# Optimization experiments

Measured on AMD Instinct MI355X. Metric: run time of the kernel, lower is better.

## Reference

```python
import jax, jax.numpy as jnp
import numpy as np

V, D, H, L, F, S, B = 32000, 1024, 16, 4, 4096, 1024, 2
THETA = 10000.0
EPS = 1e-5


def rmsnorm(x, w):
    # faithful to source: rms = sqrt(mean(x^2)) + eps (eps OUTSIDE the sqrt)
    rms = jnp.sqrt(jnp.mean(x * x, axis=-1, keepdims=True)) + EPS
    return (x / rms) * w


def rope(x, pos):
    # x: [B, H, S, dk]; rotate interleaved even/odd pairs
    dk = x.shape[-1]
    inv_freq = 1.0 / (THETA ** (jnp.arange(0, dk, 2, dtype=jnp.float32) / dk))
    ang = pos[:, None].astype(jnp.float32) * inv_freq[None, :]  # [S, dk/2]
    cos, sin = jnp.cos(ang), jnp.sin(ang)
    x1, x2 = x[..., ::2], x[..., 1::2]
    r1 = x1 * cos - x2 * sin
    r2 = x1 * sin + x2 * cos
    return jnp.stack([r1, r2], axis=-1).reshape(x.shape)


def setup_inputs() -> dict:
    key = jax.random.key(0)
    ks = jax.random.split(key, 12)
    s_attn = np.sqrt(2.0 / (D + D)).astype(np.float32)
    s_ffn = np.sqrt(2.0 / (F + D)).astype(np.float32)
    s_head = np.sqrt(2.0 / (V + D)).astype(np.float32)
    return {
        "token_ids": jax.random.randint(ks[0], (B, S), 0, V),
        "tok_emb": jax.random.normal(ks[1], (V, D), jnp.float32),
        "lm_head_w": jax.random.normal(ks[2], (V, D), jnp.float32) * s_head,
        "ln_final_w": jnp.ones((D,), jnp.float32),
        "q_w": jax.random.normal(ks[3], (L, D, D), jnp.float32) * s_attn,
        "k_w": jax.random.normal(ks[4], (L, D, D), jnp.float32) * s_attn,
        "v_w": jax.random.normal(ks[5], (L, D, D), jnp.float32) * s_attn,
        "o_w": jax.random.normal(ks[6], (L, D, D), jnp.float32) * s_attn,
        "ln1_w": jnp.ones((L, D), jnp.float32),
        "ln2_w": jnp.ones((L, D), jnp.float32),
        "w1": jax.random.normal(ks[7], (L, F, D), jnp.float32) * s_ffn,
        "w2": jax.random.normal(ks[8], (L, D, F), jnp.float32) * s_ffn,
        "w3": jax.random.normal(ks[9], (L, F, D), jnp.float32) * s_ffn,
    }


def reference(token_ids, tok_emb, lm_head_w, ln_final_w, q_w, k_w, v_w, o_w,
              ln1_w, ln2_w, w1, w2, w3):
    b, s = token_ids.shape
    dk = D // H
    scale = 1.0 / np.sqrt(dk).astype(np.float32)
    pos = jnp.arange(s)
    causal = jnp.tril(jnp.ones((s, s), dtype=bool))  # mask[i,j] = i >= j
    x = tok_emb[token_ids]  # [B, S, D]

    for l in range(L):
        # attention block with RoPE
        h = rmsnorm(x, ln1_w[l])
        q = (h @ q_w[l].T).reshape(b, s, H, dk).transpose(0, 2, 1, 3)
        k = (h @ k_w[l].T).reshape(b, s, H, dk).transpose(0, 2, 1, 3)
        v = (h @ v_w[l].T).reshape(b, s, H, dk).transpose(0, 2, 1, 3)
        q = rope(q, pos)
        k = rope(k, pos)
        scores = jnp.einsum('bhqd,bhkd->bhqk', q, k) * scale
        scores = jnp.where(causal, scores, -jnp.inf)
        attn = jax.nn.softmax(scores, axis=-1)
        o = jnp.einsum('bhqk,bhkd->bhqd', attn, v)
        o = o.transpose(0, 2, 1, 3).reshape(b, s, D)
        x = x + o @ o_w[l].T

        # SwiGLU FFN block
        h2 = rmsnorm(x, ln2_w[l])
        xw = h2 @ w1[l].T                       # [B, S, F]
        swish = xw * jax.nn.sigmoid(xw)
        x = x + (swish * (h2 @ w3[l].T)) @ w2[l].T

    x = rmsnorm(x, ln_final_w)
    return x @ lm_head_w.T  # logits [B, S, V]
```

## Files before the change

### kernel.cpp

```cpp
#include <hip/hip_runtime.h>
#include <math.h>

#define V_SZ 32000
#define D_SZ 1024
#define H_SZ 16
#define L_SZ 4
#define F_SZ 4096
#define S_SZ 1024
#define B_SZ 2
#define DK 64
#define NTOK (B_SZ * S_SZ)
#define NEG_INF -3.0e38f

typedef _Float16 half8 __attribute__((ext_vector_type(8)));
typedef _Float16 half4 __attribute__((ext_vector_type(4)));
typedef float floatx4 __attribute__((ext_vector_type(4)));

__device__ __forceinline__ void gload16(const void* g, void* l) {
    __builtin_amdgcn_global_load_lds(
        (const __attribute__((address_space(1))) unsigned int*)g,
        (__attribute__((address_space(3))) unsigned int*)l, 16, 0, 0);
}

__global__ __launch_bounds__(256) void f2h4(const float* __restrict__ s0,
                                            const float* __restrict__ s1,
                                            const float* __restrict__ s2,
                                            const float* __restrict__ s3,
                                            _Float16* __restrict__ d, int n8each) {
    const int i = blockIdx.x * 256 + threadIdx.x;
    const int sel = i / n8each;
    const int off = i - sel * n8each;
    const float* s = sel == 0 ? s0 : (sel == 1 ? s1 : (sel == 2 ? s2 : s3));
    const float4 a = ((const float4*)s)[2 * off];
    const float4 b = ((const float4*)s)[2 * off + 1];
    half8 h = {(_Float16)a.x, (_Float16)a.y, (_Float16)a.z, (_Float16)a.w,
               (_Float16)b.x, (_Float16)b.y, (_Float16)b.z, (_Float16)b.w};
    ((half8*)d)[i] = h;
}

__global__ __launch_bounds__(256) void f2h3(const float* __restrict__ s0,
                                            const float* __restrict__ s1,
                                            const float* __restrict__ s2,
                                            _Float16* __restrict__ d, int n8each) {
    const int i = blockIdx.x * 256 + threadIdx.x;
    const int sel = i / n8each;
    const int off = i - sel * n8each;
    const float* s = sel == 0 ? s0 : (sel == 1 ? s1 : s2);
    const float4 a = ((const float4*)s)[2 * off];
    const float4 b = ((const float4*)s)[2 * off + 1];
    half8 h = {(_Float16)a.x, (_Float16)a.y, (_Float16)a.z, (_Float16)a.w,
               (_Float16)b.x, (_Float16)b.y, (_Float16)b.z, (_Float16)b.w};
    ((half8*)d)[i] = h;
}

__global__ __launch_bounds__(256) void f2h(const float* __restrict__ in,
                                           _Float16* __restrict__ out, int n8) {
    const int i = blockIdx.x * 256 + threadIdx.x;
    if (i >= n8) return;
    const float4 a = ((const float4*)in)[2 * i];
    const float4 b = ((const float4*)in)[2 * i + 1];
    half8 h = {(_Float16)a.x, (_Float16)a.y, (_Float16)a.z, (_Float16)a.w,
               (_Float16)b.x, (_Float16)b.y, (_Float16)b.z, (_Float16)b.w};
    ((half8*)out)[i] = h;
}

__global__ __launch_bounds__(256) void embed_kernel(const int* __restrict__ ids,
                                                    const float* __restrict__ emb,
                                                    float* __restrict__ x) {
    const int row = blockIdx.x;
    const int id = ids[row];
    const float4* src = (const float4*)(emb + (size_t)id * D_SZ);
    float4* dst = (float4*)(x + (size_t)row * D_SZ);
    dst[threadIdx.x] = src[threadIdx.x];
}

__global__ __launch_bounds__(256) void rmsnorm_kernel(const float* __restrict__ x,
                                                      const float* __restrict__ w,
                                                      _Float16* __restrict__ out) {
    const int row = blockIdx.x;
    const int tid = threadIdx.x;
    const float4 v = ((const float4*)(x + (size_t)row * D_SZ))[tid];
    float ss = v.x * v.x + v.y * v.y + v.z * v.z + v.w * v.w;
#pragma unroll
    for (int off = 32; off > 0; off >>= 1) ss += __shfl_down(ss, off, 64);
    __shared__ float red[4];
    if ((tid & 63) == 0) red[tid >> 6] = ss;
    __syncthreads();
    const float tot = red[0] + red[1] + red[2] + red[3];
    const float inv = 1.0f / (sqrtf(tot * (1.0f / (float)D_SZ)) + 1e-5f);
    const float4 wv = ((const float4*)w)[tid];
    half4 o = {(_Float16)(v.x * inv * wv.x), (_Float16)(v.y * inv * wv.y),
               (_Float16)(v.z * inv * wv.z), (_Float16)(v.w * inv * wv.w)};
    ((half4*)(out + (size_t)row * D_SZ))[tid] = o;
}

template <int EPI, bool MFAST, int TM>
__global__ __launch_bounds__(256) void hgemm(const _Float16* __restrict__ A,
                                             const _Float16* __restrict__ B,
                                             float* __restrict__ Cf,
                                             _Float16* Ch,
                                             const _Float16* AUXh,
                                             _Float16* Cq,
                                             _Float16* Ck,
                                             _Float16* Cv,
                                             int M, int N, int K) {
    constexpr int WN = (TM == 128) ? 2 : 4;
    constexpr int CW = 128 / WN;
    constexpr int FN = CW / 16;
    __shared__ __align__(16) _Float16 As[2][TM * 32];
    __shared__ __align__(16) _Float16 Bs[2][128 * 32];
    const int tid = threadIdx.x;
    const int lane = tid & 63;
    const int wave = tid >> 6;
    const int wr = (TM == 128) ? (wave >> 1) : 0;
    const int wc = (TM == 128) ? (wave & 1) : wave;
    const int l15 = lane & 15, g = lane >> 4;

    const int gm = M / TM, gn = N >> 7, nwg = gm * gn;
    const int orig = blockIdx.x;
    const int q8 = nwg >> 3, r8 = nwg & 7, xcd = orig & 7, j8 = orig >> 3;
    const int wgid = (xcd < r8 ? xcd * (q8 + 1) : r8 * (q8 + 1) + (xcd - r8) * q8) + j8;
    const int bm = MFAST ? (wgid % gm) : (wgid / gn);
    const int bn = MFAST ? (wgid / gm) : (wgid % gn);
    const int m0 = bm * TM, n0 = bn * 128;

    const int offA0 = wave * (TM * 16) + lane * 16;
    const int offA1 = offA0 + 1024;
    const int rA0 = offA0 >> 6, kA0 = offA0 & 63;
    const int rA1 = offA1 >> 6, kA1 = offA1 & 63;
    const int offB0 = wave * 2048 + lane * 16;
    const int offB1 = offB0 + 1024;
    const int rB0 = offB0 >> 6, kB0 = offB0 & 63;
    const int rB1 = offB1 >> 6, kB1 = offB1 & 63;
    const char* gA0 = (const char*)(A + (size_t)(m0 + rA0) * K) + kA0;
    const char* gA1 = (const char*)(A + (size_t)(m0 + rA1) * K) + kA1;
    const char* gB0 = (const char*)(B + (size_t)(n0 + rB0) * K) + kB0;
    const char* gB1 = (const char*)(B + (size_t)(n0 + rB1) * K) + kB1;

#define STAGE(buf)                                                     \
    do {                                                               \
        gload16(gA0, (char*)As[buf] + offA0);                          \
        if constexpr (TM == 128) gload16(gA1, (char*)As[buf] + offA1); \
        gload16(gB0, (char*)Bs[buf] + offB0);                          \
        gload16(gB1, (char*)Bs[buf] + offB1);                          \
        gA0 += 64; gA1 += 64; gB0 += 64; gB1 += 64;                    \
    } while (0)

    floatx4 acc[4][FN];
#pragma unroll
    for (int i = 0; i < 4; i++)
#pragma unroll
        for (int j = 0; j < FN; j++) acc[i][j] = 0;

    STAGE(0);
    __syncthreads();
    int cur = 0;
    for (int kk = 0; kk < K; kk += 32) {
        if (kk + 32 < K) STAGE(cur ^ 1);
        half8 aF[4], bF[FN];
#pragma unroll
        for (int i = 0; i < 4; i++)
            aF[i] = *(const half8*)&As[cur][(wr * 64 + i * 16 + l15) * 32 + g * 8];
#pragma unroll
        for (int j = 0; j < FN; j++)
            bF[j] = *(const half8*)&Bs[cur][(wc * CW + j * 16 + l15) * 32 + g * 8];
#pragma unroll
        for (int i = 0; i < 4; i++)
#pragma unroll
            for (int j = 0; j < FN; j++)
                acc[i][j] = __builtin_amdgcn_mfma_f32_16x16x32_f16(aF[i], bF[j], acc[i][j], 0, 0, 0);
        __syncthreads();
        cur ^= 1;
    }
#undef STAGE

    const int rb = m0 + wr * 64 + g * 4;
    const int cb = n0 + wc * CW + l15;
    if (EPI == 4) {
        const int sel = n0 >> 10;
        _Float16* Cx = sel == 0 ? Cq : (sel == 1 ? Ck : Cv);
        const int cb0 = cb - sel * 1024;
#pragma unroll
        for (int i = 0; i < 4; i++) {
#pragma unroll
            for (int e = 0; e < 4; e++) {
                const int row = rb + i * 16 + e;
                const int pos = row & (S_SZ - 1);
#pragma unroll
                for (int j = 0; j < FN; j++) {
                    float v = acc[i][j][e];
                    const int col = cb0 + j * 16;
                    if (sel < 2) {
                        const float p = __shfl_xor(v, 1, 64);
                        const int pi = (col & 63) >> 1;
                        const float invf = exp2f((float)pi * -0.41524101186f);
                        float sn, cs;
                        sincosf((float)pos * invf, &sn, &cs);
                        v = (col & 1) ? (p * sn + v * cs) : (v * cs - p * sn);
                    }
                    Cx[(size_t)row * 1024 + col] = (_Float16)v;
                }
            }
        }
        return;
    }
#pragma unroll
    for (int i = 0; i < 4; i++) {
#pragma unroll
        for (int e = 0; e < 4; e++) {
            const int row = rb + i * 16 + e;
#pragma unroll
            for (int j = 0; j < FN; j++) {
                const float v = acc[i][j][e];
                if (EPI == 0) {
                    Cf[(size_t)row * N + cb + j * 16] = v;
                } else if (EPI == 1) {
                    Cf[(size_t)row * N + cb + j * 16] += v;
                } else if (EPI == 2) {
                    Ch[(size_t)row * N + cb + j * 16] =
                        (_Float16)(v / (1.0f + __expf(-v)));
                } else if (EPI == 3) {
                    const size_t idx = (size_t)row * N + cb + j * 16;
                    Ch[idx] = (_Float16)((float)AUXh[idx] * v);
                }
            }
        }
    }
}

__global__ __launch_bounds__(256) void vtrans(const _Float16* __restrict__ vh,
                                              _Float16* __restrict__ vt) {
    __shared__ __align__(16) _Float16 Ls[64][80];
    const int t = threadIdx.x;
    const int s0 = blockIdx.x * 64;
    const int bh = blockIdx.y;
    const int b = bh >> 4, h = bh & 15;
#pragma unroll
    for (int p = 0; p < 2; ++p) {
        const int sl = p * 32 + (t >> 3);
        const int d = (t & 7) * 8;
        *(half8*)&Ls[sl][d] =
            *(const half8*)&vh[((size_t)b * S_SZ + s0 + sl) * D_SZ + h * 64 + d];
    }
    __syncthreads();
#pragma unroll
    for (int p = 0; p < 2; ++p) {
        const int d = p * 32 + (t >> 3);
        const int sc = (t & 7) * 8;
        half8 v;
#pragma unroll
        for (int j = 0; j < 8; ++j) v[j] = Ls[sc + j][d];
        *(half8*)&vt[((size_t)bh * 64 + d) * S_SZ + s0 + sc] = v;
    }
}

__global__ __launch_bounds__(256) void attn_mfma(const _Float16* __restrict__ qh,
                                                 const _Float16* __restrict__ kh,
                                                 const _Float16* __restrict__ vt,
                                                 _Float16* __restrict__ o) {
    __shared__ __align__(16) _Float16 Ks[2][64 * 64];
    __shared__ __align__(16) _Float16 Vs[2][64 * 64];
    __shared__ __align__(16) _Float16 Ps[4][16][88];
    const int tid = threadIdx.x;
    const int lane = tid & 63, wave = tid >> 6;
    const int l15 = lane & 15, g = lane >> 4;
    const int bx = blockIdx.x;
    const int bh = blockIdx.y;
    const int h = bh & 15;
    const size_t tokb = (size_t)(bh >> 4) * S_SZ;

    const int qt0 = bx, qt1 = 15 - bx;
    const int qb0 = qt0 * 64, qb1 = qt1 * 64;
    const int ktmax = qt1;

    const int qrow = l15 * 4 + wave;
    half8 qA0[2], qA1[2];
#pragma unroll
    for (int kk = 0; kk < 2; ++kk) {
        qA0[kk] = *(const half8*)&qh[(tokb + qb0 + qrow) * D_SZ + h * 64 + kk * 32 + g * 8];
        qA1[kk] = *(const half8*)&qh[(tokb + qb1 + qrow) * D_SZ + h * 64 + kk * 32 + g * 8];
    }

    floatx4 accO0[4], accO1[4];
#pragma unroll
    for (int s = 0; s < 4; s++) { accO0[s] = 0; accO1[s] = 0; }
    float m0_[4] = {NEG_INF, NEG_INF, NEG_INF, NEG_INF};
    float l0_[4] = {0.0f, 0.0f, 0.0f, 0.0f};
    float m1_[4] = {NEG_INF, NEG_INF, NEG_INF, NEG_INF};
    float l1_[4] = {0.0f, 0.0f, 0.0f, 0.0f};

    const char* KbB = (const char*)(kh + tokb * D_SZ + h * 64);
    const char* VbB = (const char*)(vt + (size_t)bh * 64 * S_SZ);
    const int so0 = wave * 2048 + lane * 16;
    const int so1 = so0 + 1024;
    const int r0 = so0 >> 7, c0 = (so0 >> 4) & 7;
    const int r1 = so1 >> 7, c1 = (so1 >> 4) & 7;
    const int gc0 = ((c0 ^ (r0 & 7)) << 4);
    const int gc1 = ((c1 ^ (r1 & 7)) << 4);

#define STAGEKV(buf, kt)                                                   \
    do {                                                                   \
        const size_t kvr = (size_t)(kt) * 64;                              \
        gload16(KbB + (kvr + r0) * 2048 + gc0, (char*)Ks[buf] + so0);      \
        gload16(KbB + (kvr + r1) * 2048 + gc1, (char*)Ks[buf] + so1);      \
        gload16(VbB + r0 * 2048 + kvr * 2 + gc0, (char*)Vs[buf] + so0);    \
        gload16(VbB + r1 * 2048 + kvr * 2 + gc1, (char*)Vs[buf] + so1);    \
    } while (0)

#define LDSW(arr, rr, cc) \
    (*(const half8*)&(arr)[(rr) * 64 + ((((cc) ^ ((rr) & 7))) << 3)])

    auto computeTile = [&](const half8* qA, floatx4* accO, float* m_, float* l_,
                           int qbase, int kt, bool diag, int buf) {
        const int kv0 = kt * 64;
        floatx4 accS[4];
#pragma unroll
        for (int sub = 0; sub < 4; ++sub) {
            accS[sub] = 0;
#pragma unroll
            for (int kk = 0; kk < 2; ++kk) {
                half8 kB = LDSW(Ks[buf], sub * 16 + l15, kk * 4 + g);
                accS[sub] = __builtin_amdgcn_mfma_f32_16x16x32_f16(qA[kk], kB, accS[sub], 0, 0, 0);
            }
        }
        float sv[4][4];
        float mx[4] = {NEG_INF, NEG_INF, NEG_INF, NEG_INF};
#pragma unroll
        for (int sub = 0; sub < 4; ++sub)
#pragma unroll
            for (int e = 0; e < 4; ++e) {
                float s = accS[sub][e] * 0.125f;
                if (diag && (kv0 + sub * 16 + l15 > qbase + (g * 4 + e) * 4 + wave))
                    s = NEG_INF;
                sv[sub][e] = s;
                mx[e] = fmaxf(mx[e], s);
            }
#pragma unroll
        for (int msk = 1; msk <= 8; msk <<= 1)
#pragma unroll
            for (int e = 0; e < 4; ++e)
                mx[e] = fmaxf(mx[e], __shfl_xor(mx[e], msk, 64));
        float sf[4];
#pragma unroll
        for (int e = 0; e < 4; ++e) {
            const float mn = fmaxf(m_[e], mx[e]);
            sf[e] = __expf(m_[e] - mn);
            m_[e] = mn;
        }
        float rs[4] = {0.0f, 0.0f, 0.0f, 0.0f};
#pragma unroll
        for (int sub = 0; sub < 4; ++sub)
#pragma unroll
            for (int e = 0; e < 4; ++e) {
                const float p = __expf(sv[sub][e] - m_[e]);
                sv[sub][e] = p;
                rs[e] += p;
            }
#pragma unroll
        for (int msk = 1; msk <= 8; msk <<= 1)
#pragma unroll
            for (int e = 0; e < 4; ++e)
                rs[e] += __shfl_xor(rs[e], msk, 64);
#pragma unroll
        for (int e = 0; e < 4; ++e) l_[e] = l_[e] * sf[e] + rs[e];
#pragma unroll
        for (int sub = 0; sub < 4; ++sub)
#pragma unroll
            for (int e = 0; e < 4; ++e) accO[sub][e] *= sf[e];
#pragma unroll
        for (int sub = 0; sub < 4; ++sub)
#pragma unroll
            for (int e = 0; e < 4; ++e)
                Ps[wave][g * 4 + e][sub * 16 + l15] = (_Float16)sv[sub][e];
        half8 aP[2];
        aP[0] = *(const half8*)&Ps[wave][l15][g * 8];
        aP[1] = *(const half8*)&Ps[wave][l15][32 + g * 8];
#pragma unroll
        for (int sub = 0; sub < 4; ++sub)
#pragma unroll
            for (int kk = 0; kk < 2; ++kk) {
                half8 vB = LDSW(Vs[buf], sub * 16 + l15, kk * 4 + g);
                accO[sub] = __builtin_amdgcn_mfma_f32_16x16x32_f16(aP[kk], vB, accO[sub], 0, 0, 0);
            }
    };

    STAGEKV(0, 0);
    __syncthreads();
    int cur = 0;
    for (int kt = 0; kt <= ktmax; ++kt) {
        if (kt < ktmax) STAGEKV(cur ^ 1, kt + 1);
        computeTile(qA1, accO1, m1_, l1_, qb1, kt, kt == qt1, cur);
        if (kt <= qt0)
            computeTile(qA0, accO0, m0_, l0_, qb0, kt, kt == qt0, cur);
        __syncthreads();
        cur ^= 1;
    }
#undef STAGEKV
#undef LDSW

#pragma unroll
    for (int sub = 0; sub < 4; ++sub)
#pragma unroll
        for (int e = 0; e < 4; ++e) {
            const int rr = (g * 4 + e) * 4 + wave;
            o[(tokb + qb1 + rr) * D_SZ + h * 64 + sub * 16 + l15] =
                (_Float16)(accO1[sub][e] / l1_[e]);
            o[(tokb + qb0 + rr) * D_SZ + h * 64 + sub * 16 + l15] =
                (_Float16)(accO0[sub][e] / l0_[e]);
        }
}

extern "C" void kernel_launch(void* const* d_in, const int* in_sizes, int n_in,
                              void* d_out, int out_size, void* d_ws, size_t ws_size,
                              hipStream_t stream) {
    const int*   token_ids  = (const int*)d_in[0];
    const float* tok_emb    = (const float*)d_in[1];
    const float* lm_head_w  = (const float*)d_in[2];
    const float* ln_final_w = (const float*)d_in[3];
    const float* q_w        = (const float*)d_in[4];
    const float* k_w        = (const float*)d_in[5];
    const float* v_w        = (const float*)d_in[6];
    const float* o_w        = (const float*)d_in[7];
    const float* ln1_w      = (const float*)d_in[8];
    const float* ln2_w      = (const float*)d_in[9];
    const float* w1         = (const float*)d_in[10];
    const float* w2         = (const float*)d_in[11];
    const float* w3         = (const float*)d_in[12];
    float* out = (float*)d_out;

    char* W = (char*)d_ws;
    const size_t MB = 1u << 20;
    float*    x    = (float*)(W + 0);
    _Float16* h    = (_Float16*)(W + 8 * MB);
    _Float16* ao   = (_Float16*)(W + 12 * MB);
    _Float16* wq   = (_Float16*)(W + 16 * MB);
    _Float16* wo   = wq + 3 * (1u << 20);
    _Float16* ww1  = (_Float16*)(W + 24 * MB);
    _Float16* ww3  = ww1 + (F_SZ * D_SZ);
    _Float16* ww2  = ww3 + (F_SZ * D_SZ);
    _Float16* qh   = (_Float16*)(W + 48 * MB);
    _Float16* kh   = (_Float16*)(W + 52 * MB);
    _Float16* vh   = (_Float16*)(W + 56 * MB);
    _Float16* vt   = (_Float16*)(W + 60 * MB);
    _Float16* ff1h = (_Float16*)(W + 64 * MB);
    _Float16* whead = (_Float16*)(W + 24 * MB);

    embed_kernel<<<NTOK, 256, 0, stream>>>(token_ids, tok_emb, x);

    const int nDD8 = D_SZ * D_SZ / 8;
    const int nFD8 = F_SZ * D_SZ / 8;
    const dim3 gQKV(3 * D_SZ / 128 * (NTOK / 128));
    const dim3 gD64(D_SZ / 128 * (NTOK / 64));
    const dim3 gF(F_SZ / 128 * (NTOK / 128));
    const dim3 gATT(S_SZ / 128, B_SZ * H_SZ);
    const dim3 gVT(S_SZ / 64, B_SZ * H_SZ);

    for (int l = 0; l < L_SZ; l++) {
        const size_t oDD = (size_t)l * D_SZ * D_SZ;
        const size_t oFD = (size_t)l * F_SZ * D_SZ;
        rmsnorm_kernel<<<NTOK, 256, 0, stream>>>(x, ln1_w + (size_t)l * D_SZ, h);
        f2h4<<<4 * nDD8 / 256, 256, 0, stream>>>(q_w + oDD, k_w + oDD, v_w + oDD,
                                                 o_w + oDD, wq, nDD8);
        f2h3<<<3 * nFD8 / 256, 256, 0, stream>>>(w1 + oFD, w3 + oFD, w2 + oFD,
                                                 ww1, nFD8);
        hgemm<4, true, 128><<<gQKV, 256, 0, stream>>>(h, wq, nullptr, nullptr, nullptr,
                                                      qh, kh, vh, NTOK, 3 * D_SZ, D_SZ);
        vtrans<<<gVT, 256, 0, stream>>>(vh, vt);
        attn_mfma<<<gATT, 256, 0, stream>>>(qh, kh, vt, ao);
        hgemm<1, false, 64><<<gD64, 256, 0, stream>>>(ao, wo, x, nullptr, nullptr,
                                                      nullptr, nullptr, nullptr, NTOK, D_SZ, D_SZ);
        rmsnorm_kernel<<<NTOK, 256, 0, stream>>>(x, ln2_w + (size_t)l * D_SZ, h);
        hgemm<2, true, 128><<<gF, 256, 0, stream>>>(h, ww1, nullptr, ff1h, nullptr,
                                                    nullptr, nullptr, nullptr, NTOK, F_SZ, D_SZ);
        hgemm<3, true, 128><<<gF, 256, 0, stream>>>(h, ww3, nullptr, ff1h, ff1h,
                                                    nullptr, nullptr, nullptr, NTOK, F_SZ, D_SZ);
        hgemm<1, false, 64><<<gD64, 256, 0, stream>>>(ff1h, ww2, x, nullptr, nullptr,
                                                      nullptr, nullptr, nullptr, NTOK, D_SZ, F_SZ);
    }
    rmsnorm_kernel<<<NTOK, 256, 0, stream>>>(x, ln_final_w, h);
    const int nVD8 = V_SZ * D_SZ / 8;
    f2h<<<(nVD8 + 255) / 256, 256, 0, stream>>>(lm_head_w, whead, nVD8);
    const dim3 gOUT(V_SZ / 128 * (NTOK / 128));
    hgemm<0, true, 128><<<gOUT, 256, 0, stream>>>(h, whead, out, nullptr, nullptr,
                                                  nullptr, nullptr, nullptr, NTOK, V_SZ, D_SZ);
}
```

Measured before the change: 1.286 ms.

## Merge weight conversions, fuse W1/W3 GEMMs, add occupancy hint and MFMA priority

Merges the two per-layer fp32-to-fp16 weight conversion kernels into one launch. Runs the W1 and W3 projections as a single GEMM over the concatenated weights: the first half writes swish output, the second half writes a separate fp16 buffer, and a new elementwise kernel then multiplies them. It also adds a launch_bounds minimum-occupancy hint of 5 to the GEMM and raises wave priority around the MFMA loops in attention. The extra multiply pass adds a read and write of a 2048x4096 fp16 intermediate, and the occupancy hint may force register spills.

```diff
diff --git a/kernel.cpp b/kernel.cpp
--- a/kernel.cpp
+++ b/kernel.cpp
@@ -22,30 +22,28 @@
         (__attribute__((address_space(3))) unsigned int*)l, 16, 0, 0);
 }
 
-__global__ __launch_bounds__(256) void f2h4(const float* __restrict__ s0,
+__global__ __launch_bounds__(256) void f2h7(const float* __restrict__ sq,
+                                            const float* __restrict__ sk,
+                                            const float* __restrict__ sv,
+                                            const float* __restrict__ so,
                                             const float* __restrict__ s1,
+                                            const float* __restrict__ s3,
                                             const float* __restrict__ s2,
-                                            const float* __restrict__ s3,
-                                            _Float16* __restrict__ d, int n8each) {
+                                            _Float16* __restrict__ d,
+                                            int nDD8, int nFD8) {
     const int i = blockIdx.x * 256 + threadIdx.x;
-    const int sel = i / n8each;
-    const int off = i - sel * n8each;
-    const float* s = sel == 0 ? s0 : (sel == 1 ? s1 : (sel == 2 ? s2 : s3));
-    const float4 a = ((const float4*)s)[2 * off];
-    const float4 b = ((const float4*)s)[2 * off + 1];
-    half8 h = {(_Float16)a.x, (_Float16)a.y, (_Float16)a.z, (_Float16)a.w,
-               (_Float16)b.x, (_Float16)b.y, (_Float16)b.z, (_Float16)b.w};
-    ((half8*)d)[i] = h;
-}
-
-__global__ __launch_bounds__(256) void f2h3(const float* __restrict__ s0,
-                                            const float* __restrict__ s1,
-                                            const float* __restrict__ s2,
-                                            _Float16* __restrict__ d, int n8each) {
-    const int i = blockIdx.x * 256 + threadIdx.x;
-    const int sel = i / n8each;
-    const int off = i - sel * n8each;
-    const float* s = sel == 0 ? s0 : (sel == 1 ? s1 : s2);
+    const float* s;
+    int off;
+    if (i < 4 * nDD8) {
+        const int sel = i / nDD8;
+        off = i - sel * nDD8;
+        s = sel == 0 ? sq : (sel == 1 ? sk : (sel == 2 ? sv : so));
+    } else {
+        const int j = i - 4 * nDD8;
+        const int sel = j / nFD8;
+        off = j - sel * nFD8;
+        s = sel == 0 ? s1 : (sel == 1 ? s3 : s2);
+    }
     const float4 a = ((const float4*)s)[2 * off];
     const float4 b = ((const float4*)s)[2 * off + 1];
     half8 h = {(_Float16)a.x, (_Float16)a.y, (_Float16)a.z, (_Float16)a.w,
@@ -62,6 +60,17 @@
     half8 h = {(_Float16)a.x, (_Float16)a.y, (_Float16)a.z, (_Float16)a.w,
                (_Float16)b.x, (_Float16)b.y, (_Float16)b.z, (_Float16)b.w};
     ((half8*)out)[i] = h;
+}
+
+__global__ __launch_bounds__(256) void hmul(_Float16* __restrict__ a,
+                                            const _Float16* __restrict__ b, int n8) {
+    const int i = blockIdx.x * 256 + threadIdx.x;
+    if (i >= n8) return;
+    half8 x = ((half8*)a)[i];
+    const half8 y = ((const half8*)b)[i];
+#pragma unroll
+    for (int j = 0; j < 8; ++j) x[j] = (_Float16)((float)x[j] * (float)y[j]);
+    ((half8*)a)[i] = x;
 }
 
 __global__ __launch_bounds__(256) void embed_kernel(const int* __restrict__ ids,
@@ -95,15 +104,15 @@
 }
 
 template <int EPI, bool MFAST, int TM>
-__global__ __launch_bounds__(256) void hgemm(const _Float16* __restrict__ A,
-                                             const _Float16* __restrict__ B,
-                                             float* __restrict__ Cf,
-                                             _Float16* Ch,
-                                             const _Float16* AUXh,
-                                             _Float16* Cq,
-                                             _Float16* Ck,
-                                             _Float16* Cv,
-                                             int M, int N, int K) {
+__global__ __launch_bounds__(256, 5) void hgemm(const _Float16* __restrict__ A,
+                                                const _Float16* __restrict__ B,
+                                                float* __restrict__ Cf,
+                                                _Float16* Ch,
+                                                const _Float16* AUXh,
+                                                _Float16* Cq,
+                                                _Float16* Ck,
+                                                _Float16* Cv,
+                                                int M, int N, int K) {
     constexpr int WN = (TM == 128) ? 2 : 4;
     constexpr int CW = 128 / WN;
     constexpr int FN = CW / 16;
@@ -191,12 +200,12 @@
                     float v = acc[i][j][e];
                     const int col = cb0 + j * 16;
                     if (sel < 2) {
-                        const float p = __shfl_xor(v, 1, 64);
+                        const float pp = __shfl_xor(v, 1, 64);
                         const int pi = (col & 63) >> 1;
                         const float invf = exp2f((float)pi * -0.41524101186f);
                         float sn, cs;
                         sincosf((float)pos * invf, &sn, &cs);
-                        v = (col & 1) ? (p * sn + v * cs) : (v * cs - p * sn);
+                        v = (col & 1) ? (pp * sn + v * cs) : (v * cs - pp * sn);
                     }
                     Cx[(size_t)row * 1024 + col] = (_Float16)v;
                 }
@@ -212,16 +221,23 @@
 #pragma unroll
             for (int j = 0; j < FN; j++) {
                 const float v = acc[i][j][e];
+                const int col = cb + j * 16;
                 if (EPI == 0) {
-                    Cf[(size_t)row * N + cb + j * 16] = v;
+                    Cf[(size_t)row * N + col] = v;
                 } else if (EPI == 1) {
-                    Cf[(size_t)row * N + cb + j * 16] += v;
+                    Cf[(size_t)row * N + col] += v;
                 } else if (EPI == 2) {
-                    Ch[(size_t)row * N + cb + j * 16] =
+                    Ch[(size_t)row * N + col] =
                         (_Float16)(v / (1.0f + __expf(-v)));
                 } else if (EPI == 3) {
-                    const size_t idx = (size_t)row * N + cb + j * 16;
+                    const size_t idx = (size_t)row * N + col;
                     Ch[idx] = (_Float16)((float)AUXh[idx] * v);
+                } else if (EPI == 5) {
+                    if (col < 4096)
+                        Ch[(size_t)row * 4096 + col] =
+                            (_Float16)(v / (1.0f + __expf(-v)));
+                    else
+                        Cq[(size_t)row * 4096 + col - 4096] = (_Float16)v;
                 }
             }
         }
@@ -314,6 +330,7 @@
                            int qbase, int kt, bool diag, int buf) {
         const int kv0 = kt * 64;
         floatx4 accS[4];
+        __builtin_amdgcn_s_setprio(1);
 #pragma unroll
         for (int sub = 0; sub < 4; ++sub) {
             accS[sub] = 0;
@@ -323,6 +340,7 @@
                 accS[sub] = __builtin_amdgcn_mfma_f32_16x16x32_f16(qA[kk], kB, accS[sub], 0, 0, 0);
             }
         }
+        __builtin_amdgcn_s_setprio(0);
         float sv[4][4];
         float mx[4] = {NEG_INF, NEG_INF, NEG_INF, NEG_INF};
 #pragma unroll
@@ -375,6 +393,7 @@
         half8 aP[2];
         aP[0] = *(const half8*)&Ps[wave][l15][g * 8];
         aP[1] = *(const half8*)&Ps[wave][l15][32 + g * 8];
+        __builtin_amdgcn_s_setprio(1);
 #pragma unroll
         for (int sub = 0; sub < 4; ++sub)
 #pragma unroll
@@ -382,6 +401,7 @@
                 half8 vB = LDSW(Vs[buf], sub * 16 + l15, kk * 4 + g);
                 accO[sub] = __builtin_amdgcn_mfma_f32_16x16x32_f16(aP[kk], vB, accO[sub], 0, 0, 0);
             }
+        __builtin_amdgcn_s_setprio(0);
     };
 
     STAGEKV(0, 0);
@@ -436,12 +456,12 @@
     _Float16* wq   = (_Float16*)(W + 16 * MB);
     _Float16* wo   = wq + 3 * (1u << 20);
     _Float16* ww1  = (_Float16*)(W + 24 * MB);
-    _Float16* ww3  = ww1 + (F_SZ * D_SZ);
-    _Float16* ww2  = ww3 + (F_SZ * D_SZ);
+    _Float16* ww2  = ww1 + 2 * (F_SZ * D_SZ);
     _Float16* qh   = (_Float16*)(W + 48 * MB);
     _Float16* kh   = (_Float16*)(W + 52 * MB);
     _Float16* vh   = (_Float16*)(W + 56 * MB);
     _Float16* vt   = (_Float16*)(W + 60 * MB);
+    _Float16* ff3h = (_Float16*)(W + 48 * MB);
     _Float16* ff1h = (_Float16*)(W + 64 * MB);
     _Float16* whead = (_Float16*)(W + 24 * MB);
 
@@ -449,9 +469,10 @@
 
     const int nDD8 = D_SZ * D_SZ / 8;
     const int nFD8 = F_SZ * D_SZ / 8;
+    const int nCNV = 4 * nDD8 + 3 * nFD8;
     const dim3 gQKV(3 * D_SZ / 128 * (NTOK / 128));
     const dim3 gD64(D_SZ / 128 * (NTOK / 64));
-    const dim3 gF(F_SZ / 128 * (NTOK / 128));
+    const dim3 gW13(2 * F_SZ / 128 * (NTOK / 128));
     const dim3 gATT(S_SZ / 128, B_SZ * H_SZ);
     const dim3 gVT(S_SZ / 64, B_SZ * H_SZ);
 
@@ -459,10 +480,9 @@
         const size_t oDD = (size_t)l * D_SZ * D_SZ;
         const size_t oFD = (size_t)l * F_SZ * D_SZ;
         rmsnorm_kernel<<<NTOK, 256, 0, stream>>>(x, ln1_w + (size_t)l * D_SZ, h);
-        f2h4<<<4 * nDD8 / 256, 256, 0, stream>>>(q_w + oDD, k_w + oDD, v_w + oDD,
-                                                 o_w + oDD, wq, nDD8);
-        f2h3<<<3 * nFD8 / 256, 256, 0, stream>>>(w1 + oFD, w3 + oFD, w2 + oFD,
-                                                 ww1, nFD8);
+        f2h7<<<nCNV / 256, 256, 0, stream>>>(q_w + oDD, k_w + oDD, v_w + oDD,
+                                             o_w + oDD, w1 + oFD, w3 + oFD,
+                                             w2 + oFD, wq, nDD8, nFD8);
         hgemm<4, true, 128><<<gQKV, 256, 0, stream>>>(h, wq, nullptr, nullptr, nullptr,
                                                       qh, kh, vh, NTOK, 3 * D_SZ, D_SZ);
         vtrans<<<gVT, 256, 0, stream>>>(vh, vt);
@@ -470,10 +490,9 @@
         hgemm<1, false, 64><<<gD64, 256, 0, stream>>>(ao, wo, x, nullptr, nullptr,
                                                       nullptr, nullptr, nullptr, NTOK, D_SZ, D_SZ);
         rmsnorm_kernel<<<NTOK, 256, 0, stream>>>(x, ln2_w + (size_t)l * D_SZ, h);
-        hgemm<2, true, 128><<<gF, 256, 0, stream>>>(h, ww1, nullptr, ff1h, nullptr,
-                                                    nullptr, nullptr, nullptr, NTOK, F_SZ, D_SZ);
-        hgemm<3, true, 128><<<gF, 256, 0, stream>>>(h, ww3, nullptr, ff1h, ff1h,
-                                                    nullptr, nullptr, nullptr, NTOK, F_SZ, D_SZ);
+        hgemm<5, true, 128><<<gW13, 256, 0, stream>>>(h, ww1, nullptr, ff1h, nullptr,
+                                                      ff3h, nullptr, nullptr, NTOK, 2 * F_SZ, D_SZ);
+        hmul<<<NTOK * F_SZ / 8 / 256, 256, 0, stream>>>(ff1h, ff3h, NTOK * F_SZ / 8);
         hgemm<1, false, 64><<<gD64, 256, 0, stream>>>(ff1h, ww2, x, nullptr, nullptr,
                                                       nullptr, nullptr, nullptr, NTOK, D_SZ, F_SZ);
     }
```

Result: faster. 1.244 ms (-3.3%).
